# Optimization experiments

Hardware: AMD Instinct MI355X
Metric: run time of the kernel (lower is better)

Reference implementation:

```python
import jax, jax.numpy as jnp
import numpy as np

HID, NH, NKV, HD = 2048, 16, 8, 128
EPS = 1e-6
THETA = 10000.0
SCALE = HD ** -0.5


def setup_inputs() -> dict:
    key = jax.random.key(0)
    ks = jax.random.split(key, 6)
    S = 2048
    return {
        "positions": jnp.arange(S, dtype=jnp.int32),
        "hidden_states": jax.random.normal(ks[0], (S, HID), dtype=jnp.float32),
        "layernorm_weight": jax.random.uniform(ks[1], (HID,), dtype=jnp.float32, minval=0.5, maxval=1.5),
        "w_qkv": jax.random.normal(ks[2], ((NH + 2 * NKV) * HD, HID), dtype=jnp.float32) * 0.02,
        "w_o": jax.random.normal(ks[3], (HID, NH * HD), dtype=jnp.float32) * 0.02,
        "q_norm_w": jax.random.uniform(ks[4], (HD,), dtype=jnp.float32, minval=0.5, maxval=1.5),
        "k_norm_w": jax.random.uniform(ks[5], (HD,), dtype=jnp.float32, minval=0.5, maxval=1.5),
    }


def _rmsnorm(x, w, eps=EPS):
    var = jnp.mean(jnp.square(x), axis=-1, keepdims=True)
    return x * jax.lax.rsqrt(var + eps) * w


def _rope(x, cos, sin):
    # x: [S, h, HD]; cos/sin: [S, 1, HD//2] (neox-style rotate-half)
    x1, x2 = x[..., : HD // 2], x[..., HD // 2 :]
    return jnp.concatenate([x1 * cos - x2 * sin, x2 * cos + x1 * sin], axis=-1)


def reference(positions, hidden_states, layernorm_weight, w_qkv, w_o, q_norm_w, k_norm_w):
    S = hidden_states.shape[0]
    # Fused RMSNorm + QKV projection
    hn = _rmsnorm(hidden_states, layernorm_weight)
    qkv = hn @ w_qkv.T  # [S, (NH+2*NKV)*HD]
    q, k, v = jnp.split(qkv, [NH * HD, (NH + NKV) * HD], axis=-1)
    q = q.reshape(S, NH, HD)
    k = k.reshape(S, NKV, HD)
    v = v.reshape(S, NKV, HD)
    # Per-head QK RMSNorm
    q = _rmsnorm(q, q_norm_w)
    k = _rmsnorm(k, k_norm_w)
    # RoPE
    inv_freq = 1.0 / (THETA ** (jnp.arange(0, HD, 2, dtype=jnp.float32) / HD))
    freqs = positions.astype(jnp.float32)[:, None] * inv_freq  # [S, HD//2]
    cos = jnp.cos(freqs)[:, None, :]
    sin = jnp.sin(freqs)[:, None, :]
    q = _rope(q, cos, sin)
    k = _rope(k, cos, sin)
    # GQA: expand kv heads to match query heads
    rep = NH // NKV
    k = jnp.repeat(k, rep, axis=1)  # [S, NH, HD]
    v = jnp.repeat(v, rep, axis=1)
    # Causal attention
    scores = jnp.einsum("shd,thd->hst", q, k) * SCALE  # [NH, S, S]
    causal = jnp.tril(jnp.ones((S, S), dtype=bool))
    scores = jnp.where(causal, scores, jnp.finfo(scores.dtype).min)
    probs = jax.nn.softmax(scores, axis=-1)
    out = jnp.einsum("hst,thd->shd", probs, v)  # [S, NH, HD]
    # Output projection
    return out.reshape(S, NH * HD) @ w_o.T
```

## Files before the change

### kernel.cpp

```cpp
#include <hip/hip_runtime.h>
#include <hip/hip_bf16.h>
#include <math.h>

#define HID 2048
#define NH 16
#define NKV 8
#define HD 128
#define SEQ 2048
#define EPS 1e-6f
#define THETA 10000.0f
#define SCALE 0.08838834764831845f
#define DTHR 90.50966799187809f

typedef __attribute__((ext_vector_type(8))) short bf8_t;
typedef __attribute__((ext_vector_type(4))) short bf4_t;
typedef __attribute__((ext_vector_type(4))) float f4_t;

__device__ __forceinline__ short f2bf(float f) {
    union { __hip_bfloat16 h; short s; } u;
    u.h = __float2bfloat16(f);
    return u.s;
}
__device__ __forceinline__ float bf2f(short s) {
    union { short s; __hip_bfloat16 h; } u;
    u.s = s;
    return __bfloat162float(u.h);
}
__device__ __forceinline__ bf8_t pack8(const float4& a, const float4& b) {
    bf8_t r;
    r[0] = f2bf(a.x); r[1] = f2bf(a.y); r[2] = f2bf(a.z); r[3] = f2bf(a.w);
    r[4] = f2bf(b.x); r[5] = f2bf(b.y); r[6] = f2bf(b.z); r[7] = f2bf(b.w);
    return r;
}
__device__ __forceinline__ void gload16(const short* g, short* l) {
    __builtin_amdgcn_global_load_lds(
        (const __attribute__((address_space(1))) unsigned int*)g,
        (__attribute__((address_space(3))) unsigned int*)l, 16, 0, 0);
}

__device__ __forceinline__ float wave_reduce_sum(float v) {
#pragma unroll
    for (int off = 32; off > 0; off >>= 1) v += __shfl_xor(v, off);
    return v;
}

__global__ __launch_bounds__(256) void prep_kernel(
    const float* __restrict__ w_qkv, short* __restrict__ wqb,
    const float* __restrict__ w_o, short* __restrict__ wob,
    const float* __restrict__ x, const float* __restrict__ w,
    short* __restrict__ out) {
    int bid = blockIdx.x;
    int tid = threadIdx.x;
    if (bid < 4096) {
        int i = bid * 256 + tid;
        float4 a = *(const float4*)(w_qkv + (size_t)i * 8);
        float4 b = *(const float4*)(w_qkv + (size_t)i * 8 + 4);
        *(bf8_t*)(wqb + (size_t)i * 8) = pack8(a, b);
        return;
    }
    if (bid < 6144) {
        int i = (bid - 4096) * 256 + tid;
        float4 a = *(const float4*)(w_o + (size_t)i * 8);
        float4 b = *(const float4*)(w_o + (size_t)i * 8 + 4);
        *(bf8_t*)(wob + (size_t)i * 8) = pack8(a, b);
        return;
    }
    int row = bid - 6144;
    const float* xr = x + (size_t)row * HID;
    float4 a = *(const float4*)(xr + tid * 8);
    float4 b = *(const float4*)(xr + tid * 8 + 4);
    float ss = a.x * a.x + a.y * a.y + a.z * a.z + a.w * a.w +
               b.x * b.x + b.y * b.y + b.z * b.z + b.w * b.w;
    ss = wave_reduce_sum(ss);
    __shared__ float part[4];
    __shared__ float s_scale;
    if ((tid & 63) == 0) part[tid >> 6] = ss;
    __syncthreads();
    if (tid == 0) {
        float t = part[0] + part[1] + part[2] + part[3];
        s_scale = rsqrtf(t / (float)HID + EPS);
    }
    __syncthreads();
    float sc = s_scale;
    float4 wa = *(const float4*)(w + tid * 8);
    float4 wb = *(const float4*)(w + tid * 8 + 4);
    float4 oa = make_float4(a.x * sc * wa.x, a.y * sc * wa.y,
                            a.z * sc * wa.z, a.w * sc * wa.w);
    float4 ob = make_float4(b.x * sc * wb.x, b.y * sc * wb.y,
                            b.z * sc * wb.z, b.w * sc * wb.w);
    *(bf8_t*)(out + (size_t)row * HID + tid * 8) = pack8(oa, ob);
}

template <int MODE>
__global__ __launch_bounds__(256) void gemm_mfma_kernel(
    const short* __restrict__ A, const short* __restrict__ B,
    float* __restrict__ C0, float* __restrict__ C1,
    short* __restrict__ Q, short* __restrict__ Kp,
    short* __restrict__ Vr, int M, int N, int K) {
    __shared__ short As[128][64];
    __shared__ short Bs[128][64];
    int tid = threadIdx.x;
    int wv = tid >> 6, lane = tid & 63;
    int n16 = lane & 15, qd = lane >> 4;
    int m0 = blockIdx.y * 128, n0 = blockIdx.x * 128;
    int wm = (wv >> 1) * 64, wn = (wv & 1) * 64;
    int sr8 = lane >> 3, slot = lane & 7;

    int kbeg, kend;
    float* Cf;
    if (MODE == 0) {
        int z = blockIdx.z;
        kbeg = z ? (K >> 1) : 0;
        kend = z ? K : (K >> 1);
        Cf = z ? C1 : C0;
    } else {
        kbeg = 0; kend = K; Cf = nullptr;
    }

    size_t ainv[4], binv[4];
#pragma unroll
    for (int it = 0; it < 4; ++it) {
        int row = wv * 32 + it * 8 + sr8;
        int chunk = (slot - row) & 7;
        ainv[it] = (size_t)(m0 + row) * K + chunk * 8;
        binv[it] = (size_t)(n0 + row) * K + chunk * 8;
    }

    f4_t acc[4][4];
#pragma unroll
    for (int i = 0; i < 4; ++i)
#pragma unroll
        for (int j = 0; j < 4; ++j) acc[i][j] = (f4_t){0.f, 0.f, 0.f, 0.f};

    for (int k0 = kbeg; k0 < kend; k0 += 64) {
        __syncthreads();
#pragma unroll
        for (int it = 0; it < 4; ++it) {
            gload16(A + ainv[it] + k0, &As[wv * 32 + it * 8][0]);
            gload16(B + binv[it] + k0, &Bs[wv * 32 + it * 8][0]);
        }
        __syncthreads();

        bf8_t af[4][2], bf[4][2];
#pragma unroll
        for (int t = 0; t < 4; ++t)
#pragma unroll
            for (int ks = 0; ks < 2; ++ks) {
                int ar = wm + t * 16 + n16;
                af[t][ks] = *(const bf8_t*)&As[ar][(((ks * 4 + qd) + ar) & 7) * 8];
                int br = wn + t * 16 + n16;
                bf[t][ks] = *(const bf8_t*)&Bs[br][(((ks * 4 + qd) + br) & 7) * 8];
            }
#pragma unroll
        for (int ks = 0; ks < 2; ++ks)
#pragma unroll
            for (int mt = 0; mt < 4; ++mt)
#pragma unroll
                for (int nt = 0; nt < 4; ++nt)
                    acc[mt][nt] = __builtin_amdgcn_mfma_f32_16x16x32_bf16(
                        af[mt][ks], bf[nt][ks], acc[mt][nt], 0, 0, 0);
    }

#pragma unroll
    for (int mt = 0; mt < 4; ++mt)
#pragma unroll
        for (int nt = 0; nt < 4; ++nt)
#pragma unroll
            for (int r = 0; r < 4; ++r) {
                int gm = m0 + wm + mt * 16 + qd * 4 + r;
                int gn = n0 + wn + nt * 16 + n16;
                float v = acc[mt][nt][r];
                if (MODE == 0) {
                    Cf[(size_t)gm * N + gn] = v;
                } else {
                    if (gn < NH * HD)
                        Q[(size_t)gm * (NH * HD) + gn] = f2bf(v);
                    else if (gn < (NH + NKV) * HD)
                        Kp[(size_t)gm * (NKV * HD) + (gn - NH * HD)] = f2bf(v);
                    else
                        Vr[(size_t)gm * (NKV * HD) + (gn - (NH + NKV) * HD)] = f2bf(v);
                }
            }
}

__global__ __launch_bounds__(256) void splitk_reduce_kernel(
    const float* __restrict__ p0, const float* __restrict__ p1,
    float* __restrict__ o) {
    size_t i = ((size_t)blockIdx.x * 256 + threadIdx.x) * 8;
    float4 a0 = *(const float4*)(p0 + i);
    float4 a1 = *(const float4*)(p0 + i + 4);
    float4 b0 = *(const float4*)(p1 + i);
    float4 b1 = *(const float4*)(p1 + i + 4);
    *(float4*)(o + i) =
        make_float4(a0.x + b0.x, a0.y + b0.y, a0.z + b0.z, a0.w + b0.w);
    *(float4*)(o + i + 4) =
        make_float4(a1.x + b1.x, a1.y + b1.y, a1.z + b1.z, a1.w + b1.w);
}

__global__ __launch_bounds__(256) void mid_kernel(
    const short* __restrict__ vr, short* __restrict__ vt,
    short* __restrict__ q, short* __restrict__ k,
    const float* __restrict__ qw, const float* __restrict__ kw,
    const int* __restrict__ pos) {
    int bid = blockIdx.x;
    int tid = threadIdx.x;
    if (bid < 512) {
        __shared__ short t[64][64];
        int s0 = (bid & 31) * 64, d0 = (bid >> 5) * 64;
        int sl = tid >> 3, ch = tid & 7;
#pragma unroll
        for (int it = 0; it < 2; ++it) {
            int s_local = it * 32 + sl;
            bf8_t vv = *(const bf8_t*)(vr + (size_t)(s0 + s_local) * (NKV * HD) + d0 + ch * 8);
            *(bf8_t*)&t[s_local][((ch + s_local) & 7) * 8] = vv;
        }
        __syncthreads();
#pragma unroll
        for (int it = 0; it < 2; ++it) {
            int d_local = it * 32 + sl;
            int sbase = ch * 8;
            bf8_t o;
#pragma unroll
            for (int j = 0; j < 8; ++j) {
                int s = sbase + j;
                o[j] = t[s][(((d_local >> 3) + s) & 7) * 8 + (d_local & 7)];
            }
            *(bf8_t*)(vt + (size_t)(d0 + d_local) * SEQ + s0 + sbase) = o;
        }
        return;
    }
    int u = (bid - 512) * 2 + (tid >> 7);
    int ui = tid >> 7, d = tid & 127;
    int s = u / 24, hh = u % 24;
    short* ptr;
    const float* w;
    if (hh < NH) {
        ptr = q + (size_t)s * (NH * HD) + hh * HD;
        w = qw;
    } else {
        ptr = k + (size_t)s * (NKV * HD) + (hh - NH) * HD;
        w = kw;
    }
    float x = bf2f(ptr[d]);
    float ss = wave_reduce_sum(x * x);
    __shared__ float part[2][2];
    if ((d & 63) == 0) part[ui][d >> 6] = ss;
    __syncthreads();
    float tot = part[ui][0] + part[ui][1];
    float xn = x * rsqrtf(tot / (float)HD + EPS) * w[d];
    __shared__ float sh[2][HD];
    sh[ui][d] = xn;
    __syncthreads();
    int j = d & 63;
    float inv = __expf((float)j * -0.14391156831f);
    float fr = (float)pos[s] * inv;
    float sn, cs;
    __sincosf(fr, &sn, &cs);
    float o;
    if (d < 64)
        o = xn * cs - sh[ui][d + 64] * sn;
    else
        o = xn * cs + sh[ui][d - 64] * sn;
    ptr[d] = f2bf(o);
}

__device__ __forceinline__ void attn_stage(
    short (&kb)[64][128], short (&vb)[128][64],
    const short* __restrict__ kg, const short* __restrict__ vg,
    int t0, const int (&kinv)[4], const int (&vinv)[4], int wv) {
#pragma unroll
    for (int it = 0; it < 4; ++it) {
        gload16(kg + (size_t)t0 * (NKV * HD) + kinv[it], &kb[wv * 16 + it * 4][0]);
        gload16(vg + t0 + vinv[it], &vb[wv * 32 + it * 8][0]);
    }
}

__device__ __forceinline__ void attn_tile(
    const short (&kb)[64][128], const short (&vb)[128][64],
    short (&psh)[4][2][16][64],
    const bf8_t (&qf)[2][4], f4_t (&of)[2][8],
    float (&m_i)[2], float (&l_p)[2],
    int wv, int n, int qd, int koff) {
    f4_t sc[2][4];
#pragma unroll
    for (int g = 0; g < 2; ++g)
#pragma unroll
        for (int kk = 0; kk < 4; ++kk) sc[g][kk] = (f4_t){0.f, 0.f, 0.f, 0.f};
    __builtin_amdgcn_s_setprio(1);
#pragma unroll
    for (int kk = 0; kk < 4; ++kk) {
        int key = kk * 16 + n;
#pragma unroll
        for (int ks = 0; ks < 4; ++ks) {
            bf8_t kf = *(const bf8_t*)&kb[key][(((ks * 4 + qd) + key) & 15) * 8];
            sc[0][kk] = __builtin_amdgcn_mfma_f32_16x16x32_bf16(kf, qf[0][ks], sc[0][kk], 0, 0, 0);
            sc[1][kk] = __builtin_amdgcn_mfma_f32_16x16x32_bf16(kf, qf[1][ks], sc[1][kk], 0, 0, 0);
        }
    }
    __builtin_amdgcn_s_setprio(0);
#pragma unroll
    for (int g = 0; g < 2; ++g) {
        int rows0 = wv * 32 + g * 16;
        int qrow = rows0 + n;
        if (koff + 63 > rows0) {
#pragma unroll
            for (int kk = 0; kk < 4; ++kk)
#pragma unroll
                for (int r = 0; r < 4; ++r)
                    if (koff + kk * 16 + qd * 4 + r > qrow) sc[g][kk][r] = -1e30f;
        }
        float m01 = fmaxf(fmaxf(fmaxf(sc[g][0][0], sc[g][0][1]), fmaxf(sc[g][0][2], sc[g][0][3])),
                          fmaxf(fmaxf(sc[g][1][0], sc[g][1][1]), fmaxf(sc[g][1][2], sc[g][1][3])));
        float m23 = fmaxf(fmaxf(fmaxf(sc[g][2][0], sc[g][2][1]), fmaxf(sc[g][2][2], sc[g][2][3])),
                          fmaxf(fmaxf(sc[g][3][0], sc[g][3][1]), fmaxf(sc[g][3][2], sc[g][3][3])));
        float mx = fmaxf(m01, m23);
        mx = fmaxf(mx, __shfl_xor(mx, 16));
        mx = fmaxf(mx, __shfl_xor(mx, 32));
        if (!__all(mx <= m_i[g] + DTHR)) {
            float mnew = fmaxf(m_i[g], mx);
            float al = __expf((m_i[g] - mnew) * SCALE);
            m_i[g] = mnew;
            l_p[g] *= al;
#pragma unroll
            for (int r = 0; r < 4; ++r) {
                float alr = __shfl(al, qd * 4 + r);
#pragma unroll
                for (int nb = 0; nb < 8; ++nb) of[g][nb][r] *= alr;
            }
        }
        float mcur = m_i[g];
        float lsum = 0.f;
#pragma unroll
        for (int kk = 0; kk < 4; ++kk) {
            bf4_t pk;
#pragma unroll
            for (int r = 0; r < 4; ++r) {
                float p = __expf((sc[g][kk][r] - mcur) * SCALE);
                lsum += p;
                pk[r] = f2bf(p);
            }
            *(bf4_t*)&psh[wv][g][n][(kk * 16 + qd * 4 + n * 8) & 63] = pk;
        }
        l_p[g] += lsum;
    }
    __builtin_amdgcn_wave_barrier();
    __builtin_amdgcn_s_setprio(1);
#pragma unroll
    for (int ks2 = 0; ks2 < 2; ++ks2) {
        bf8_t pf0 = *(const bf8_t*)&psh[wv][0][n][((ks2 * 32 + qd * 8) + n * 8) & 63];
        bf8_t pf1 = *(const bf8_t*)&psh[wv][1][n][((ks2 * 32 + qd * 8) + n * 8) & 63];
#pragma unroll
        for (int nb = 0; nb < 8; ++nb) {
            int dim = nb * 16 + n;
            bf8_t vf = *(const bf8_t*)&vb[dim][(((ks2 * 4 + qd) + dim) & 7) * 8];
            of[0][nb] = __builtin_amdgcn_mfma_f32_16x16x32_bf16(pf0, vf, of[0][nb], 0, 0, 0);
            of[1][nb] = __builtin_amdgcn_mfma_f32_16x16x32_bf16(pf1, vf, of[1][nb], 0, 0, 0);
        }
    }
    __builtin_amdgcn_s_setprio(0);
}

__global__ __launch_bounds__(256, 2) void attn_chunk_kernel(
    const short* __restrict__ q, const short* __restrict__ k,
    const short* __restrict__ vt, short* __restrict__ opart,
    float* __restrict__ ml) {
    __shared__ short kbufA[64][128], kbufB[64][128];
    __shared__ short vbufA[128][64], vbufB[128][64];
    __shared__ short psh[4][2][16][64];

    int tid = threadIdx.x;
    int wv = tid >> 6, lane = tid & 63;
    int n = lane & 15, qd = lane >> 4;

    int i = blockIdx.x;
    int hs = i >> 8, p = i & 255;
    int h = p >> 4;
    int qt = hs ? (p & 15) : (15 - (p & 15));
    int c = hs;
    int qbase = qt * 128;
    int tstart = c ? (qt + 1) : 0;
    int tcount = qt + 1;
    int kvh = h >> 1;

    int kinv[4], vinv[4];
#pragma unroll
    for (int it = 0; it < 4; ++it) {
        int key = wv * 16 + it * 4 + (lane >> 4);
        int ck = ((lane & 15) - key) & 15;
        kinv[it] = key * (NKV * HD) + kvh * HD + ck * 8;
        int dim = wv * 32 + it * 8 + (lane >> 3);
        int cv = ((lane & 7) - dim) & 7;
        vinv[it] = (kvh * HD + dim) * SEQ + cv * 8;
    }

    bf8_t qf[2][4];
#pragma unroll
    for (int g = 0; g < 2; ++g) {
        const short* qp =
            q + (size_t)(qbase + wv * 32 + g * 16 + n) * (NH * HD) + h * HD + qd * 8;
#pragma unroll
        for (int ks = 0; ks < 4; ++ks) qf[g][ks] = *(const bf8_t*)(qp + ks * 32);
    }

    f4_t of[2][8];
#pragma unroll
    for (int g = 0; g < 2; ++g)
#pragma unroll
        for (int x = 0; x < 8; ++x) of[g][x] = (f4_t){0.f, 0.f, 0.f, 0.f};
    float m_i[2] = {-1e30f, -1e30f};
    float l_p[2] = {0.f, 0.f};

    attn_stage(kbufA, vbufA, k, vt, tstart * 64, kinv, vinv, wv);
    for (int tt = 0; tt < tcount; tt += 2) {
        __syncthreads();
        if (tt + 1 < tcount)
            attn_stage(kbufB, vbufB, k, vt, (tstart + tt + 1) * 64, kinv, vinv, wv);
        attn_tile(kbufA, vbufA, psh, qf, of, m_i, l_p, wv, n, qd,
                  (tstart + tt) * 64 - qbase);
        if (tt + 1 < tcount) {
            __syncthreads();
            if (tt + 2 < tcount)
                attn_stage(kbufA, vbufA, k, vt, (tstart + tt + 2) * 64, kinv, vinv, wv);
            attn_tile(kbufB, vbufB, psh, qf, of, m_i, l_p, wv, n, qd,
                      (tstart + tt + 1) * 64 - qbase);
        }
    }

    float lred[2];
#pragma unroll
    for (int g = 0; g < 2; ++g) {
        float l = l_p[g];
        l += __shfl_xor(l, 16);
        l += __shfl_xor(l, 32);
        lred[g] = l;
    }

    size_t pb = ((size_t)(h * 16 + qt)) * 2 + c;
    short* op = opart + pb * (128 * 128);
#pragma unroll
    for (int g = 0; g < 2; ++g)
#pragma unroll
        for (int nb = 0; nb < 8; ++nb)
#pragma unroll
            for (int r = 0; r < 4; ++r) {
                int rl = wv * 32 + g * 16 + qd * 4 + r;
                op[rl * 128 + nb * 16 + n] = f2bf(of[g][nb][r]);
            }
    if (qd == 0) {
#pragma unroll
        for (int g = 0; g < 2; ++g) {
            int rl = wv * 32 + g * 16 + n;
            ml[pb * 256 + rl * 2] = m_i[g] * SCALE;
            ml[pb * 256 + rl * 2 + 1] = lred[g];
        }
    }
}

__global__ __launch_bounds__(256) void attn_merge_kernel(
    const short* __restrict__ opart, const float* __restrict__ ml,
    short* __restrict__ o) {
    int bid = blockIdx.x;
    int h = bid >> 4, qt = bid & 15;
    int tid = threadIdx.x;
    int r = tid >> 1, hf = tid & 1;
    size_t pb0 = ((size_t)(h * 16 + qt)) * 2;
    size_t pb1 = pb0 + 1;
    float m0 = ml[pb0 * 256 + r * 2], l0 = ml[pb0 * 256 + r * 2 + 1];
    float m1 = ml[pb1 * 256 + r * 2], l1 = ml[pb1 * 256 + r * 2 + 1];
    float M = fmaxf(m0, m1);
    float w0 = __expf(m0 - M), w1 = __expf(m1 - M);
    float invL = 1.0f / (w0 * l0 + w1 * l1);
    int row = qt * 128 + r;
#pragma unroll
    for (int j = 0; j < 8; ++j) {
        int d0 = hf * 64 + j * 8;
        bf8_t a = *(const bf8_t*)(opart + pb0 * (128 * 128) + r * 128 + d0);
        bf8_t b = *(const bf8_t*)(opart + pb1 * (128 * 128) + r * 128 + d0);
        bf8_t e;
#pragma unroll
        for (int x = 0; x < 8; ++x)
            e[x] = f2bf((w0 * bf2f(a[x]) + w1 * bf2f(b[x])) * invL);
        *(bf8_t*)(o + (size_t)row * (NH * HD) + h * HD + d0) = e;
    }
}

extern "C" void kernel_launch(void* const* d_in, const int* in_sizes, int n_in,
                              void* d_out, int out_size, void* d_ws, size_t ws_size,
                              hipStream_t stream) {
    const int* positions   = (const int*)d_in[0];
    const float* hidden    = (const float*)d_in[1];
    const float* ln_w      = (const float*)d_in[2];
    const float* w_qkv     = (const float*)d_in[3];
    const float* w_o       = (const float*)d_in[4];
    const float* q_norm_w  = (const float*)d_in[5];
    const float* k_norm_w  = (const float*)d_in[6];
    float* out = (float*)d_out;

    char* base = (char*)d_ws;
    short* hnb   = (short*)(base);
    short* wqb   = (short*)(base + ((size_t)8 << 20));
    short* vtb   = (short*)(base + ((size_t)8 << 20));
    float* mlbuf = (float*)(base + ((size_t)12 << 20));
    short* wob   = (short*)(base + ((size_t)24 << 20));
    short* qbf   = (short*)(base + ((size_t)32 << 20));
    short* kbf   = (short*)(base + ((size_t)40 << 20));
    short* vrow  = (short*)(base + ((size_t)44 << 20));
    short* opart = (short*)d_out;
    float* p0 = (float*)(base + ((size_t)8 << 20));
    float* p1 = (float*)(base + ((size_t)32 << 20));

    prep_kernel<<<8192, 256, 0, stream>>>(w_qkv, wqb, w_o, wob, hidden, ln_w, hnb);
    gemm_mfma_kernel<1><<<dim3(32, 16), 256, 0, stream>>>(
        hnb, wqb, nullptr, nullptr, qbf, kbf, vrow, SEQ, (NH + 2 * NKV) * HD, HID);
    mid_kernel<<<512 + 24576, 256, 0, stream>>>(
        vrow, vtb, qbf, kbf, q_norm_w, k_norm_w, positions);
    attn_chunk_kernel<<<512, 256, 0, stream>>>(qbf, kbf, vtb, opart, mlbuf);
    attn_merge_kernel<<<256, 256, 0, stream>>>(opart, mlbuf, hnb);
    gemm_mfma_kernel<0><<<dim3(16, 16, 2), 256, 0, stream>>>(
        hnb, wob, p0, p1, nullptr, nullptr, nullptr, SEQ, NH * HD, HID);
    splitk_reduce_kernel<<<2048, 256, 0, stream>>>(p0, p1, out);
}
```

Baseline: 259.4 us.

## Split-K the QKV GEMM into two bf16 partials summed in mid_kernel

The QKV projection GEMM is launched with a z-dimension of 2, so each half of K writes a bf16 partial result into a separate 4096-wide buffer (one partial lives in the output buffer). mid_kernel now reads both partials and adds them before the QK RMSNorm/RoPE and before the V transpose, so no separate reduction kernel is needed. This doubles the block count of the QKV GEMM to improve occupancy across CUs. The cost is extra partial-buffer traffic, and the rounding of each partial to bf16 before summing loses precision. The workspace layout is reshuffled to fit the new buffers.

```diff
diff --git a/kernel.cpp b/kernel.cpp
--- a/kernel.cpp
+++ b/kernel.cpp
@@ -106,16 +106,13 @@
     int wm = (wv >> 1) * 64, wn = (wv & 1) * 64;
     int sr8 = lane >> 3, slot = lane & 7;
 
-    int kbeg, kend;
-    float* Cf;
-    if (MODE == 0) {
-        int z = blockIdx.z;
-        kbeg = z ? (K >> 1) : 0;
-        kend = z ? K : (K >> 1);
-        Cf = z ? C1 : C0;
-    } else {
-        kbeg = 0; kend = K; Cf = nullptr;
-    }
+    int z = blockIdx.z;
+    int kbeg = z ? (K >> 1) : 0;
+    int kend = z ? K : (K >> 1);
+    float* Cf = nullptr;
+    short* Pp = nullptr;
+    if (MODE == 0) Cf = z ? C1 : C0;
+    else           Pp = z ? Kp : Q;
 
     size_t ainv[4], binv[4];
 #pragma unroll
@@ -170,16 +167,8 @@
                 int gm = m0 + wm + mt * 16 + qd * 4 + r;
                 int gn = n0 + wn + nt * 16 + n16;
                 float v = acc[mt][nt][r];
-                if (MODE == 0) {
-                    Cf[(size_t)gm * N + gn] = v;
-                } else {
-                    if (gn < NH * HD)
-                        Q[(size_t)gm * (NH * HD) + gn] = f2bf(v);
-                    else if (gn < (NH + NKV) * HD)
-                        Kp[(size_t)gm * (NKV * HD) + (gn - NH * HD)] = f2bf(v);
-                    else
-                        Vr[(size_t)gm * (NKV * HD) + (gn - (NH + NKV) * HD)] = f2bf(v);
-                }
+                if (MODE == 0) Cf[(size_t)gm * N + gn] = v;
+                else           Pp[(size_t)gm * N + gn] = f2bf(v);
             }
 }
 
@@ -198,8 +187,8 @@
 }
 
 __global__ __launch_bounds__(256) void mid_kernel(
-    const short* __restrict__ vr, short* __restrict__ vt,
-    short* __restrict__ q, short* __restrict__ k,
+    const short* __restrict__ pA, const short* __restrict__ pB,
+    short* __restrict__ vt, short* __restrict__ q, short* __restrict__ k,
     const float* __restrict__ qw, const float* __restrict__ kw,
     const int* __restrict__ pos) {
     int bid = blockIdx.x;
@@ -211,7 +200,12 @@
 #pragma unroll
         for (int it = 0; it < 2; ++it) {
             int s_local = it * 32 + sl;
-            bf8_t vv = *(const bf8_t*)(vr + (size_t)(s0 + s_local) * (NKV * HD) + d0 + ch * 8);
+            size_t off = (size_t)(s0 + s_local) * 4096 + 3072 + d0 + ch * 8;
+            bf8_t a = *(const bf8_t*)(pA + off);
+            bf8_t b = *(const bf8_t*)(pB + off);
+            bf8_t vv;
+#pragma unroll
+            for (int j = 0; j < 8; ++j) vv[j] = f2bf(bf2f(a[j]) + bf2f(b[j]));
             *(bf8_t*)&t[s_local][((ch + s_local) & 7) * 8] = vv;
         }
         __syncthreads();
@@ -232,16 +226,20 @@
     int u = (bid - 512) * 2 + (tid >> 7);
     int ui = tid >> 7, d = tid & 127;
     int s = u / 24, hh = u % 24;
-    short* ptr;
+    int col;
+    short* optr;
     const float* w;
     if (hh < NH) {
-        ptr = q + (size_t)s * (NH * HD) + hh * HD;
+        col = hh * HD + d;
+        optr = q + (size_t)s * (NH * HD) + hh * HD;
         w = qw;
     } else {
-        ptr = k + (size_t)s * (NKV * HD) + (hh - NH) * HD;
+        col = 2048 + (hh - NH) * HD + d;
+        optr = k + (size_t)s * (NKV * HD) + (hh - NH) * HD;
         w = kw;
     }
-    float x = bf2f(ptr[d]);
+    size_t poff = (size_t)s * 4096 + col;
+    float x = bf2f(pA[poff]) + bf2f(pB[poff]);
     float ss = wave_reduce_sum(x * x);
     __shared__ float part[2][2];
     if ((d & 63) == 0) part[ui][d >> 6] = ss;
@@ -261,7 +259,7 @@
         o = xn * cs - sh[ui][d + 64] * sn;
     else
         o = xn * cs + sh[ui][d - 64] * sn;
-    ptr[d] = f2bf(o);
+    optr[d] = f2bf(o);
 }
 
 __device__ __forceinline__ void attn_stage(
@@ -499,21 +497,22 @@
     char* base = (char*)d_ws;
     short* hnb   = (short*)(base);
     short* wqb   = (short*)(base + ((size_t)8 << 20));
-    short* vtb   = (short*)(base + ((size_t)8 << 20));
-    float* mlbuf = (float*)(base + ((size_t)12 << 20));
+    short* qbf   = (short*)(base + ((size_t)8 << 20));
+    short* kbf   = (short*)(base + ((size_t)16 << 20));
+    short* vtb   = (short*)(base + ((size_t)20 << 20));
     short* wob   = (short*)(base + ((size_t)24 << 20));
-    short* qbf   = (short*)(base + ((size_t)32 << 20));
-    short* kbf   = (short*)(base + ((size_t)40 << 20));
-    short* vrow  = (short*)(base + ((size_t)44 << 20));
+    short* pB    = (short*)(base + ((size_t)32 << 20));
+    float* mlbuf = (float*)(base + ((size_t)48 << 20));
+    short* pA    = (short*)d_out;
     short* opart = (short*)d_out;
-    float* p0 = (float*)(base + ((size_t)8 << 20));
-    float* p1 = (float*)(base + ((size_t)32 << 20));
+    float* p0    = (float*)(base + ((size_t)8 << 20));
+    float* p1    = (float*)(base + ((size_t)32 << 20));
 
     prep_kernel<<<8192, 256, 0, stream>>>(w_qkv, wqb, w_o, wob, hidden, ln_w, hnb);
-    gemm_mfma_kernel<1><<<dim3(32, 16), 256, 0, stream>>>(
-        hnb, wqb, nullptr, nullptr, qbf, kbf, vrow, SEQ, (NH + 2 * NKV) * HD, HID);
+    gemm_mfma_kernel<1><<<dim3(32, 16, 2), 256, 0, stream>>>(
+        hnb, wqb, nullptr, nullptr, pA, pB, nullptr, SEQ, (NH + 2 * NKV) * HD, HID);
     mid_kernel<<<512 + 24576, 256, 0, stream>>>(
-        vrow, vtb, qbf, kbf, q_norm_w, k_norm_w, positions);
+        pA, pB, vtb, qbf, kbf, q_norm_w, k_norm_w, positions);
     attn_chunk_kernel<<<512, 256, 0, stream>>>(qbf, kbf, vtb, opart, mlbuf);
     attn_merge_kernel<<<256, 256, 0, stream>>>(opart, mlbuf, hnb);
     gemm_mfma_kernel<0><<<dim3(16, 16, 2), 256, 0, stream>>>(
```

Result: no change. 260.9 us (+0.6%).
